# Optimization experiments

Measured on AMD Instinct MI355X. Metric: run time of the kernel, lower is better.

## Reference

```python
import jax, jax.numpy as jnp
import numpy as np

WSCALE = 0.05  # keep ReLU MLP activations in a sane range


def setup_inputs() -> dict:
    key = jax.random.key(0)
    ks = jax.random.split(key, 9)
    B, D, H = 2048, 64, 512
    return {
        "x": jax.random.normal(ks[0], (B, D), dtype=jnp.float32),
        "W1": jax.random.normal(ks[1], (H, D), dtype=jnp.float32) * WSCALE,
        "b1": jax.random.normal(ks[2], (H,), dtype=jnp.float32) * WSCALE,
        "W2": jax.random.normal(ks[3], (H, H), dtype=jnp.float32) * WSCALE,
        "b2": jax.random.normal(ks[4], (H,), dtype=jnp.float32) * WSCALE,
        "W3": jax.random.normal(ks[5], (H, H), dtype=jnp.float32) * WSCALE,
        "b3": jax.random.normal(ks[6], (H,), dtype=jnp.float32) * WSCALE,
        "W4": jax.random.normal(ks[7], (D, H), dtype=jnp.float32) * WSCALE,
        "b4": jax.random.normal(ks[8], (D,), dtype=jnp.float32) * WSCALE,
    }


def reference(x, W1, b1, W2, b2, W3, b3, W4, b4):
    # Score network: ReLU MLP (weights stored PyTorch-style [out, in]).
    a1 = x @ W1.T + b1          # [B, H]
    h1 = jax.nn.relu(a1)
    a2 = h1 @ W2.T + b2
    h2 = jax.nn.relu(a2)
    a3 = h2 @ W3.T + b3
    h3 = jax.nn.relu(a3)
    s = h3 @ W4.T + b4          # [B, D] score

    # Divergence = trace of Jacobian ds/dx per sample.
    # Per-sample J = W4 @ diag(m3) @ W3 @ diag(m2) @ W2 @ diag(m1) @ W1,
    # with m_k = 1[a_k > 0] (ReLU derivative; 0 at 0 like torch autograd).
    m1 = (a1 > 0).astype(x.dtype)
    m2 = (a2 > 0).astype(x.dtype)
    m3 = (a3 > 0).astype(x.dtype)
    T = m1[:, :, None] * W1[None, :, :]                 # [B, H, D]
    T = m2[:, :, None] * jnp.einsum('ij,bjd->bid', W2, T)  # [B, H, D]
    T = m3[:, :, None] * jnp.einsum('ij,bjd->bid', W3, T)  # [B, H, D]
    div = jnp.einsum('dj,bjd->b', W4, T)                # trace of J, [B]

    # Hyvarinen score: 0.5 * ||s||^2 + div
    val = 0.5 * jnp.sum(s * s, axis=1) + div
    return val
```

## Files before the change

### kernel.cpp

```cpp
#include <hip/hip_runtime.h>
#include <stdint.h>


typedef __attribute__((ext_vector_type(8))) short short8;
typedef __attribute__((ext_vector_type(4))) float f32x4;

union U16x8 {
  uint4 u;
  short8 s;
};

__device__ __forceinline__ uint16_t f2bf(float f) {
  uint32_t u = __float_as_uint(f);
  uint32_t lsb = (u >> 16) & 1u;
  u += 0x7FFFu + lsb;
  return (uint16_t)(u >> 16);
}

__device__ __forceinline__ void lds_load16(const uint4* gsrc, uint4* ldst) {
  __builtin_amdgcn_global_load_lds(
      (const __attribute__((address_space(1))) void*)gsrc,
      (__attribute__((address_space(3))) void*)ldst, 16, 0, 0);
}

__global__ __launch_bounds__(256) void convert_kernel(
    const float* __restrict__ W1, const float* __restrict__ W2,
    const float* __restrict__ W3, const float* __restrict__ W4,
    uint16_t* __restrict__ A2swz, uint16_t* __restrict__ A3swz,
    uint16_t* __restrict__ B1swz, uint16_t* __restrict__ B4swz,
    float* __restrict__ W2Tf, float* __restrict__ W3Tf,
    float* __restrict__ W1Tf, float* __restrict__ W4Tf) {
  const int i = blockIdx.x * 256 + threadIdx.x;
  if (i < 262144) {
    const int e = i;
    const int f = e >> 3, j = e & 7;
    const int lane = f & 63, fk = f >> 6;
    const int kc = fk & 15, r16 = fk >> 4;
    const int l15 = lane & 15, quad = lane >> 4;
    const int row = r16 * 16 + l15, col = kc * 32 + quad * 8 + j;
    A2swz[e] = f2bf(W2[row * 512 + col]);
  } else if (i < 524288) {
    const int e = i - 262144;
    const int f = e >> 3, j = e & 7;
    const int lane = f & 63, fk = f >> 6;
    const int kc = fk & 15, r16 = fk >> 4;
    const int l15 = lane & 15, quad = lane >> 4;
    const int row = r16 * 16 + l15, col = kc * 32 + quad * 8 + j;
    A3swz[e] = f2bf(W3[col * 512 + row]);
  } else if (i < 557056) {
    const int e = i - 524288;
    const int f = e >> 3, j = e & 7;
    const int lane = f & 63, fk = f >> 6;
    const int kc = fk >> 2, jt = fk & 3;
    const int l15 = lane & 15, quad = lane >> 4;
    const int d = jt * 16 + l15, col = kc * 32 + quad * 8 + j;
    B1swz[e] = f2bf(W1[col * 64 + d]);
  } else if (i < 589824) {
    const int e = i - 557056;
    const int f = e >> 3, j = e & 7;
    const int lane = f & 63, fk = f >> 6;
    const int kc = fk >> 2, jt = fk & 3;
    const int l15 = lane & 15, quad = lane >> 4;
    const int d = jt * 16 + l15, col = kc * 32 + quad * 8 + j;
    B4swz[e] = f2bf(W4[d * 512 + col]);
  } else if (i < 851968) {
    const int e = i - 589824;
    const int k = e >> 9, jj = e & 511;
    W2Tf[e] = W2[jj * 512 + k];
  } else if (i < 1114112) {
    const int e = i - 851968;
    const int k = e >> 9, jj = e & 511;
    W3Tf[e] = W3[jj * 512 + k];
  } else if (i < 1146880) {
    const int e = i - 1114112;
    const int k = e >> 9, jj = e & 511;
    W1Tf[e] = W1[jj * 64 + k];
  } else if (i < 1179648) {
    const int e = i - 1146880;
    const int k = e >> 6, d = e & 63;
    W4Tf[e] = W4[d * 512 + k];
  }
}

__device__ __forceinline__ float4 frelu4(float a0, float a1, float a2, float a3) {
  float4 r;
  r.x = a0 > 0.f ? a0 : 0.f;
  r.y = a1 > 0.f ? a1 : 0.f;
  r.z = a2 > 0.f ? a2 : 0.f;
  r.w = a3 > 0.f ? a3 : 0.f;
  return r;
}

template <int KPW>
__device__ __forceinline__ void fwd_layer8(
    const float* __restrict__ WT, const float* __restrict__ bias,
    const float4* __restrict__ src, float4* __restrict__ dst,
    float4 (* __restrict__ pa)[512], uint32_t* __restrict__ mbase,
    int t, int lane, int kh) {
  float acc[8][4];
#pragma unroll
  for (int p = 0; p < 8; ++p)
#pragma unroll
    for (int s = 0; s < 4; ++s) acc[p][s] = 0.f;

  const int k0 = kh * KPW;
  const float* Wb = WT + (size_t)k0 * 512 + lane;
  float wA[8], wB[8];
#pragma unroll
  for (int p = 0; p < 8; ++p) wA[p] = Wb[p * 64];
  float4 hA_ = src[k0];

#pragma unroll 1
  for (int kk = 0; kk < KPW; kk += 2) {
    const float4 hB_ = src[k0 + kk + 1];
#pragma unroll
    for (int p = 0; p < 8; ++p) wB[p] = Wb[(size_t)(kk + 1) * 512 + p * 64];
#pragma unroll
    for (int p = 0; p < 8; ++p) {
      acc[p][0] = fmaf(wA[p], hA_.x, acc[p][0]);
      acc[p][1] = fmaf(wA[p], hA_.y, acc[p][1]);
      acc[p][2] = fmaf(wA[p], hA_.z, acc[p][2]);
      acc[p][3] = fmaf(wA[p], hA_.w, acc[p][3]);
    }
    hA_ = src[k0 + kk + 2];
#pragma unroll
    for (int p = 0; p < 8; ++p) wA[p] = Wb[(size_t)(kk + 2) * 512 + p * 64];
#pragma unroll
    for (int p = 0; p < 8; ++p) {
      acc[p][0] = fmaf(wB[p], hB_.x, acc[p][0]);
      acc[p][1] = fmaf(wB[p], hB_.y, acc[p][1]);
      acc[p][2] = fmaf(wB[p], hB_.z, acc[p][2]);
      acc[p][3] = fmaf(wB[p], hB_.w, acc[p][3]);
    }
  }

#pragma unroll
  for (int p = 0; p < 8; ++p) {
    float4 v;
    v.x = acc[p][0]; v.y = acc[p][1]; v.z = acc[p][2]; v.w = acc[p][3];
    pa[kh][p * 64 + lane] = v;
  }
  __syncthreads();

#pragma unroll
  for (int pass = 0; pass < 2; ++pass) {
    const int u = pass * 256 + t;
    const float4 a0 = pa[0][u], a1 = pa[1][u], a2 = pa[2][u], a3 = pa[3][u];
    const float bj = bias[u];
    float a[4];
    a[0] = ((a0.x + a1.x) + (a2.x + a3.x)) + bj;
    a[1] = ((a0.y + a1.y) + (a2.y + a3.y)) + bj;
    a[2] = ((a0.z + a1.z) + (a2.z + a3.z)) + bj;
    a[3] = ((a0.w + a1.w) + (a2.w + a3.w)) + bj;
#pragma unroll
    for (int s = 0; s < 4; ++s) {
      const unsigned long long bal = __ballot(a[s] > 0.f);
      if (lane == 0) {
        uint2 w2;
        w2.x = (uint32_t)bal;
        w2.y = (uint32_t)(bal >> 32);
        *(uint2*)(mbase + (size_t)s * 16 + pass * 8 + 2 * kh) = w2;
      }
    }
    dst[u] = frelu4(a[0], a[1], a[2], a[3]);
  }
  __syncthreads();
}

__global__ __launch_bounds__(256) void forward_kernel(
    const float* __restrict__ x,
    const float* __restrict__ W1Tf, const float* __restrict__ b1,
    const float* __restrict__ W2Tf, const float* __restrict__ b2,
    const float* __restrict__ W3Tf, const float* __restrict__ b3,
    const float* __restrict__ W4Tf, const float* __restrict__ b4,
    uint32_t* __restrict__ m1p, uint32_t* __restrict__ m2p,
    uint32_t* __restrict__ m3p, float* __restrict__ out) {
  __shared__ float4 xs[64];
  __shared__ float4 hU[512];
  __shared__ float4 hV[512];
  __shared__ float4 pa[4][512];
  const int t = threadIdx.x;
  const int lane = t & 63, kh = t >> 6;
  const int b0 = blockIdx.x * 4;

  {
    const int k2 = t >> 2, s2 = t & 3;
    ((float*)&xs[k2])[s2] = x[(size_t)(b0 + s2) * 64 + k2];
  }
  __syncthreads();

  fwd_layer8<16>(W1Tf, b1, xs, hU, pa, m1p + (size_t)b0 * 16, t, lane, kh);
  fwd_layer8<128>(W2Tf, b2, hU, hV, pa, m2p + (size_t)b0 * 16, t, lane, kh);
  fwd_layer8<128>(W3Tf, b3, hV, hU, pa, m3p + (size_t)b0 * 16, t, lane, kh);

  {
    const int d = lane;
    const int k0 = kh * 128;
    const float* Wb = W4Tf + (size_t)k0 * 64 + d;
    float a4[4] = {0.f, 0.f, 0.f, 0.f};
    float wA = Wb[0], wB;
    float4 hA_ = hU[k0], hB_;
#pragma unroll 1
    for (int kk = 0; kk < 128; kk += 2) {
      hB_ = hU[k0 + kk + 1];
      wB = Wb[(size_t)(kk + 1) * 64];
      a4[0] = fmaf(wA, hA_.x, a4[0]); a4[1] = fmaf(wA, hA_.y, a4[1]);
      a4[2] = fmaf(wA, hA_.z, a4[2]); a4[3] = fmaf(wA, hA_.w, a4[3]);
      hA_ = hU[k0 + kk + 2];
      wA = Wb[(size_t)(kk + 2) * 64];
      a4[0] = fmaf(wB, hB_.x, a4[0]); a4[1] = fmaf(wB, hB_.y, a4[1]);
      a4[2] = fmaf(wB, hB_.z, a4[2]); a4[3] = fmaf(wB, hB_.w, a4[3]);
    }
    float4 v;
    v.x = a4[0]; v.y = a4[1]; v.z = a4[2]; v.w = a4[3];
    pa[kh][d] = v;
  }
  __syncthreads();
  if (t < 64) {
    const float4 q0 = pa[0][t], q1 = pa[1][t], q2 = pa[2][t], q3 = pa[3][t];
    const float bj = b4[t];
    float sq[4];
    sq[0] = ((q0.x + q1.x) + (q2.x + q3.x)) + bj;
    sq[1] = ((q0.y + q1.y) + (q2.y + q3.y)) + bj;
    sq[2] = ((q0.z + q1.z) + (q2.z + q3.z)) + bj;
    sq[3] = ((q0.w + q1.w) + (q2.w + q3.w)) + bj;
#pragma unroll
    for (int s = 0; s < 4; ++s) sq[s] *= sq[s];
#pragma unroll
    for (int off = 32; off; off >>= 1) {
      sq[0] += __shfl_down(sq[0], off, 64);
      sq[1] += __shfl_down(sq[1], off, 64);
      sq[2] += __shfl_down(sq[2], off, 64);
      sq[3] += __shfl_down(sq[3], off, 64);
    }
    if (t == 0) {
      out[b0 + 0] = 0.5f * sq[0];
      out[b0 + 1] = 0.5f * sq[1];
      out[b0 + 2] = 0.5f * sq[2];
      out[b0 + 3] = 0.5f * sq[3];
    }
  }
}

__device__ __forceinline__ void expand_mask(uint32_t byte8, uint32_t mk[4]) {
#pragma unroll
  for (int i = 0; i < 4; ++i) {
    mk[i] = (((byte8 >> (2 * i)) & 1u) ? 0x0000FFFFu : 0u) |
            (((byte8 >> (2 * i + 1)) & 1u) ? 0xFFFF0000u : 0u);
  }
}

__global__ __launch_bounds__(512, 4) void div_kernel(
    const uint4* __restrict__ A2swz, const uint4* __restrict__ A3swz,
    const uint4* __restrict__ B1swz, const uint4* __restrict__ B4swz,
    const uint32_t* __restrict__ m1p, const uint32_t* __restrict__ m2p,
    const uint32_t* __restrict__ m3p, float* __restrict__ out) {
  __shared__ uint4 sfrag[3][16][64];
  __shared__ uint4 emask[8][16][4];
  const int t = threadIdx.x;
  const int lane = t & 63, wv = t >> 6;
  const int quad = lane >> 4, l15 = lane & 15;
  const int g4 = blockIdx.x;
  const int rowB0 = blockIdx.y * 64;
  const int sLoc = wv & 3;
  const int b = g4 * 4 + sLoc;
  const int r16b = blockIdx.y * 4;
  const bool isC = (wv < 4);

  const uint4* sb = (wv < 2) ? A2swz : (wv < 4) ? B1swz : (wv < 6) ? A3swz : B4swz;

  f32x4 acc[4][4];
#pragma unroll
  for (int it = 0; it < 4; ++it)
#pragma unroll
    for (int jt = 0; jt < 4; ++jt) acc[it][jt] = (f32x4){0.f, 0.f, 0.f, 0.f};

  {
    const uint32_t* mp = (isC ? m1p : m3p) + (size_t)b * 16;
    const int kcl = lane >> 2, qd = lane & 3;
    const uint32_t word = mp[kcl];
    uint32_t mk[4];
    expand_mask((word >> (qd * 8)) & 0xFFu, mk);
    uint4 v;
    v.x = mk[0]; v.y = mk[1]; v.z = mk[2]; v.w = mk[3];
    emask[wv][kcl][qd] = v;
  }

  auto stage = [&](int sbuf, int kc) {
#pragma unroll
    for (int q = 0; q < 2; ++q) {
      const int sub = (wv & 1) * 2 + q;
      const size_t off = ((wv & 2) == 0)
          ? ((size_t)((r16b + sub) * 16 + kc) * 64 + lane)
          : ((size_t)(kc * 4 + sub) * 64 + lane);
      lds_load16(sb + off, &sfrag[sbuf][wv * 2 + q][0]);
    }
  };

  stage(0, 0);
  stage(1, 1);
  __builtin_amdgcn_sched_barrier(0);
  asm volatile("s_waitcnt vmcnt(2)" ::: "memory");
  __builtin_amdgcn_s_barrier();
  __builtin_amdgcn_sched_barrier(0);

  const int base = isC ? 0 : 8;

#pragma unroll 1
  for (int kc = 0; kc < 16; ++kc) {
    const int rb = kc % 3;
    if (kc < 14) stage((kc + 2) % 3, kc + 2);

    const uint4 mku = emask[wv][kc][quad];

    uint4 a[4], u[4];
#pragma unroll
    for (int q = 0; q < 4; ++q) {
      a[q] = sfrag[rb][base + q][lane];
      u[q] = sfrag[rb][base + 4 + q][lane];
    }

    short8 bf[4];
#pragma unroll
    for (int jt = 0; jt < 4; ++jt) {
      U16x8 uu;
      uu.u = u[jt];
      uu.u.x &= mku.x; uu.u.y &= mku.y; uu.u.z &= mku.z; uu.u.w &= mku.w;
      bf[jt] = uu.s;
    }
#pragma unroll
    for (int it = 0; it < 4; ++it) {
      U16x8 ua;
      ua.u = a[it];
      const short8 af = ua.s;
#pragma unroll
      for (int jt = 0; jt < 4; ++jt)
        acc[it][jt] = __builtin_amdgcn_mfma_f32_16x16x32_bf16(af, bf[jt], acc[it][jt], 0, 0, 0);
    }

    if (kc < 14) {
      asm volatile("s_waitcnt vmcnt(2)" ::: "memory");
    } else if (kc == 14) {
      asm volatile("s_waitcnt vmcnt(0)" ::: "memory");
    }
    if (kc < 15) {
      __builtin_amdgcn_s_barrier();
      __builtin_amdgcn_sched_barrier(0);
    }
  }

  __syncthreads();
  float* cxf = (float*)&sfrag[0][0][0];
  float dsum = 0.f;
  const uint32_t* m2w = m2p + (size_t)b * 16;
#pragma unroll
  for (int h = 0; h < 2; ++h) {
    if (isC) {
#pragma unroll
      for (int ith = 0; ith < 2; ++ith)
#pragma unroll
        for (int jt = 0; jt < 4; ++jt) {
          float* crow = &cxf[((size_t)sLoc * 32 + ith * 16 + quad * 4) * 65 +
                             jt * 16 + l15];
          crow[0 * 65] = acc[h * 2 + ith][jt][0];
          crow[1 * 65] = acc[h * 2 + ith][jt][1];
          crow[2 * 65] = acc[h * 2 + ith][jt][2];
          crow[3 * 65] = acc[h * 2 + ith][jt][3];
        }
    }
    __syncthreads();
    if (!isC) {
#pragma unroll
      for (int ith = 0; ith < 2; ++ith) {
        const int it = h * 2 + ith;
        const int rloc = it * 16 + quad * 4;
        const uint32_t md = m2w[(rowB0 + rloc) >> 5];
        const uint32_t bits = (md >> (rloc & 31)) & 0xFu;
        const float w0 = (bits & 1u) ? 1.f : 0.f;
        const float w1 = (bits & 2u) ? 1.f : 0.f;
        const float w2 = (bits & 4u) ? 1.f : 0.f;
        const float w3 = (bits & 8u) ? 1.f : 0.f;
#pragma unroll
        for (int jt = 0; jt < 4; ++jt) {
          const float* crow = &cxf[((size_t)sLoc * 32 + ith * 16 + quad * 4) * 65 +
                                   jt * 16 + l15];
          dsum = fmaf(w0, acc[it][jt][0] * crow[0 * 65], dsum);
          dsum = fmaf(w1, acc[it][jt][1] * crow[1 * 65], dsum);
          dsum = fmaf(w2, acc[it][jt][2] * crow[2 * 65], dsum);
          dsum = fmaf(w3, acc[it][jt][3] * crow[3 * 65], dsum);
        }
      }
    }
    __syncthreads();
  }
  if (!isC) {
#pragma unroll
    for (int off = 32; off; off >>= 1) dsum += __shfl_down(dsum, off, 64);
    if (lane == 0) atomicAdd(out + b, dsum);
  }
}

extern "C" void kernel_launch(void* const* d_in, const int* in_sizes, int n_in,
                              void* d_out, int out_size, void* d_ws, size_t ws_size,
                              hipStream_t stream) {
  const float* x  = (const float*)d_in[0];
  const float* W1 = (const float*)d_in[1];
  const float* b1 = (const float*)d_in[2];
  const float* W2 = (const float*)d_in[3];
  const float* b2 = (const float*)d_in[4];
  const float* W3 = (const float*)d_in[5];
  const float* b3 = (const float*)d_in[6];
  const float* W4 = (const float*)d_in[7];
  const float* b4 = (const float*)d_in[8];
  float* out = (float*)d_out;

  char* ws = (char*)d_ws;
  uint16_t* A2swz = (uint16_t*)(ws + 0);
  uint16_t* A3swz = (uint16_t*)(ws + 524288);
  uint16_t* B1swz = (uint16_t*)(ws + 1048576);
  uint16_t* B4swz = (uint16_t*)(ws + 1114112);
  float*    W2Tf  = (float*)(ws + 1179648);
  float*    W3Tf  = (float*)(ws + 2228224);
  float*    W1Tf  = (float*)(ws + 3276800);
  float*    W4Tf  = (float*)(ws + 3407872);
  uint32_t* m1p   = (uint32_t*)(ws + 3538944);
  uint32_t* m2p   = (uint32_t*)(ws + 3670016);
  uint32_t* m3p   = (uint32_t*)(ws + 3801088);
  if (ws_size < 3932160) return;

  convert_kernel<<<4608, 256, 0, stream>>>(W1, W2, W3, W4,
                                           A2swz, A3swz, B1swz, B4swz,
                                           W2Tf, W3Tf, W1Tf, W4Tf);
  forward_kernel<<<512, 256, 0, stream>>>(x, W1Tf, b1, W2Tf, b2, W3Tf, b3,
                                          W4Tf, b4, m1p, m2p, m3p, out);
  div_kernel<<<dim3(512, 8), 512, 0, stream>>>((const uint4*)A2swz,
                                               (const uint4*)A3swz,
                                               (const uint4*)B1swz,
                                               (const uint4*)B4swz,
                                               m1p, m2p, m3p, out);
}
```

Measured before the change: 264.4 us.

## Split forward MLP K-reduction across eight waves per block with deeper prefetch

```diff
diff --git a/kernel.cpp b/kernel.cpp
--- a/kernel.cpp
+++ b/kernel.cpp
@@ -82,70 +82,84 @@
   }
 }
 
-__device__ __forceinline__ float4 frelu4(float a0, float a1, float a2, float a3) {
-  float4 r;
-  r.x = a0 > 0.f ? a0 : 0.f;
-  r.y = a1 > 0.f ? a1 : 0.f;
-  r.z = a2 > 0.f ? a2 : 0.f;
-  r.w = a3 > 0.f ? a3 : 0.f;
-  return r;
+__device__ __forceinline__ void fma8x4(float acc[8][4], const float w[8],
+                                       const float4 h) {
+#pragma unroll
+  for (int p = 0; p < 8; ++p) {
+    acc[p][0] = fmaf(w[p], h.x, acc[p][0]);
+    acc[p][1] = fmaf(w[p], h.y, acc[p][1]);
+    acc[p][2] = fmaf(w[p], h.z, acc[p][2]);
+    acc[p][3] = fmaf(w[p], h.w, acc[p][3]);
+  }
 }
 
 template <int KPW>
-__device__ __forceinline__ void fwd_layer8(
+__device__ __forceinline__ void fwd_layer9(
     const float* __restrict__ WT, const float* __restrict__ bias,
     const float4* __restrict__ src, float4* __restrict__ dst,
-    float4 (* __restrict__ pa)[512], uint32_t* __restrict__ mbase,
-    int t, int lane, int kh) {
+    float4 (* __restrict__ pah)[512], uint32_t* __restrict__ mbase,
+    int t, int lane, int wv) {
   float acc[8][4];
 #pragma unroll
   for (int p = 0; p < 8; ++p)
 #pragma unroll
     for (int s = 0; s < 4; ++s) acc[p][s] = 0.f;
 
-  const int k0 = kh * KPW;
+  const int k0 = wv * KPW;
   const float* Wb = WT + (size_t)k0 * 512 + lane;
-  float wA[8], wB[8];
-#pragma unroll
-  for (int p = 0; p < 8; ++p) wA[p] = Wb[p * 64];
-  float4 hA_ = src[k0];
+  float w0[8], w1[8], w2[8], w3[8];
+#pragma unroll
+  for (int p = 0; p < 8; ++p) {
+    w0[p] = Wb[(size_t)0 * 512 + p * 64];
+    w1[p] = Wb[(size_t)1 * 512 + p * 64];
+    w2[p] = Wb[(size_t)2 * 512 + p * 64];
+    w3[p] = Wb[(size_t)3 * 512 + p * 64];
+  }
+  float4 h0 = src[k0 + 0], h1 = src[k0 + 1], h2 = src[k0 + 2], h3 = src[k0 + 3];
 
 #pragma unroll 1
-  for (int kk = 0; kk < KPW; kk += 2) {
-    const float4 hB_ = src[k0 + kk + 1];
-#pragma unroll
-    for (int p = 0; p < 8; ++p) wB[p] = Wb[(size_t)(kk + 1) * 512 + p * 64];
+  for (int kk = 0; kk < KPW; kk += 4) {
+    fma8x4(acc, w0, h0);
+    h0 = src[k0 + kk + 4];
+#pragma unroll
+    for (int p = 0; p < 8; ++p) w0[p] = Wb[(size_t)(kk + 4) * 512 + p * 64];
+    fma8x4(acc, w1, h1);
+    h1 = src[k0 + kk + 5];
+#pragma unroll
+    for (int p = 0; p < 8; ++p) w1[p] = Wb[(size_t)(kk + 5) * 512 + p * 64];
+    fma8x4(acc, w2, h2);
+    h2 = src[k0 + kk + 6];
+#pragma unroll
+    for (int p = 0; p < 8; ++p) w2[p] = Wb[(size_t)(kk + 6) * 512 + p * 64];
+    fma8x4(acc, w3, h3);
+    h3 = src[k0 + kk + 7];
+#pragma unroll
+    for (int p = 0; p < 8; ++p) w3[p] = Wb[(size_t)(kk + 7) * 512 + p * 64];
+  }
+
+  const int half = wv >> 1;
+  if ((wv & 1) == 0) {
 #pragma unroll
     for (int p = 0; p < 8; ++p) {
-      acc[p][0] = fmaf(wA[p], hA_.x, acc[p][0]);
-      acc[p][1] = fmaf(wA[p], hA_.y, acc[p][1]);
-      acc[p][2] = fmaf(wA[p], hA_.z, acc[p][2]);
-      acc[p][3] = fmaf(wA[p], hA_.w, acc[p][3]);
-    }
-    hA_ = src[k0 + kk + 2];
-#pragma unroll
-    for (int p = 0; p < 8; ++p) wA[p] = Wb[(size_t)(kk + 2) * 512 + p * 64];
+      float4 v;
+      v.x = acc[p][0]; v.y = acc[p][1]; v.z = acc[p][2]; v.w = acc[p][3];
+      pah[half][p * 64 + lane] = v;
+    }
+  }
+  __syncthreads();
+  if (wv & 1) {
 #pragma unroll
     for (int p = 0; p < 8; ++p) {
-      acc[p][0] = fmaf(wB[p], hB_.x, acc[p][0]);
-      acc[p][1] = fmaf(wB[p], hB_.y, acc[p][1]);
-      acc[p][2] = fmaf(wB[p], hB_.z, acc[p][2]);
-      acc[p][3] = fmaf(wB[p], hB_.w, acc[p][3]);
-    }
-  }
-
-#pragma unroll
-  for (int p = 0; p < 8; ++p) {
-    float4 v;
-    v.x = acc[p][0]; v.y = acc[p][1]; v.z = acc[p][2]; v.w = acc[p][3];
-    pa[kh][p * 64 + lane] = v;
+      float4 v = pah[half][p * 64 + lane];
+      v.x += acc[p][0]; v.y += acc[p][1]; v.z += acc[p][2]; v.w += acc[p][3];
+      pah[half][p * 64 + lane] = v;
+    }
   }
   __syncthreads();
 
-#pragma unroll
-  for (int pass = 0; pass < 2; ++pass) {
-    const int u = pass * 256 + t;
-    const float4 a0 = pa[0][u], a1 = pa[1][u], a2 = pa[2][u], a3 = pa[3][u];
+  {
+    const int u = t;
+    const float4 a0 = pah[0][u], a1 = pah[1][u], a2 = pah[2][u], a3 = pah[3][u];
     const float bj = bias[u];
     float a[4];
     a[0] = ((a0.x + a1.x) + (a2.x + a3.x)) + bj;
@@ -156,18 +170,23 @@
     for (int s = 0; s < 4; ++s) {
       const unsigned long long bal = __ballot(a[s] > 0.f);
       if (lane == 0) {
-        uint2 w2;
-        w2.x = (uint32_t)bal;
-        w2.y = (uint32_t)(bal >> 32);
-        *(uint2*)(mbase + (size_t)s * 16 + pass * 8 + 2 * kh) = w2;
+        uint2 w2v;
+        w2v.x = (uint32_t)bal;
+        w2v.y = (uint32_t)(bal >> 32);
+        *(uint2*)(mbase + (size_t)s * 16 + 2 * wv) = w2v;
       }
     }
-    dst[u] = frelu4(a[0], a[1], a[2], a[3]);
+    float4 r;
+    r.x = a[0] > 0.f ? a[0] : 0.f;
+    r.y = a[1] > 0.f ? a[1] : 0.f;
+    r.z = a[2] > 0.f ? a[2] : 0.f;
+    r.w = a[3] > 0.f ? a[3] : 0.f;
+    dst[u] = r;
   }
   __syncthreads();
 }
 
-__global__ __launch_bounds__(256) void forward_kernel(
+__global__ __launch_bounds__(512, 4) void forward_kernel(
     const float* __restrict__ x,
     const float* __restrict__ W1Tf, const float* __restrict__ b1,
     const float* __restrict__ W2Tf, const float* __restrict__ b2,
@@ -178,46 +197,62 @@
   __shared__ float4 xs[64];
   __shared__ float4 hU[512];
   __shared__ float4 hV[512];
-  __shared__ float4 pa[4][512];
+  __shared__ float4 pah[4][512];
   const int t = threadIdx.x;
-  const int lane = t & 63, kh = t >> 6;
+  const int lane = t & 63, wv = t >> 6;
   const int b0 = blockIdx.x * 4;
 
-  {
+  if (t < 256) {
     const int k2 = t >> 2, s2 = t & 3;
     ((float*)&xs[k2])[s2] = x[(size_t)(b0 + s2) * 64 + k2];
   }
   __syncthreads();
 
-  fwd_layer8<16>(W1Tf, b1, xs, hU, pa, m1p + (size_t)b0 * 16, t, lane, kh);
-  fwd_layer8<128>(W2Tf, b2, hU, hV, pa, m2p + (size_t)b0 * 16, t, lane, kh);
-  fwd_layer8<128>(W3Tf, b3, hV, hU, pa, m3p + (size_t)b0 * 16, t, lane, kh);
+  fwd_layer9<8>(W1Tf, b1, xs, hU, pah, m1p + (size_t)b0 * 16, t, lane, wv);
+  fwd_layer9<64>(W2Tf, b2, hU, hV, pah, m2p + (size_t)b0 * 16, t, lane, wv);
+  fwd_layer9<64>(W3Tf, b3, hV, hU, pah, m3p + (size_t)b0 * 16, t, lane, wv);
 
   {
     const int d = lane;
-    const int k0 = kh * 128;
-    const float* Wb = W4Tf + (size_t)k0 * 64 + d;
+    const int k0 = wv * 64;
+    const float* Wb4 = W4Tf + (size_t)k0 * 64 + d;
     float a4[4] = {0.f, 0.f, 0.f, 0.f};
-    float wA = Wb[0], wB;
-    float4 hA_ = hU[k0], hB_;
+    float v0 = Wb4[(size_t)0 * 64], v1 = Wb4[(size_t)1 * 64];
+    float v2 = Wb4[(size_t)2 * 64], v3 = Wb4[(size_t)3 * 64];
+    float4 g0 = hU[k0 + 0], g1 = hU[k0 + 1], g2 = hU[k0 + 2], g3 = hU[k0 + 3];
 #pragma unroll 1
-    for (int kk = 0; kk < 128; kk += 2) {
-      hB_ = hU[k0 + kk + 1];
-      wB = Wb[(size_t)(kk + 1) * 64];
-      a4[0] = fmaf(wA, hA_.x, a4[0]); a4[1] = fmaf(wA, hA_.y, a4[1]);
-      a4[2] = fmaf(wA, hA_.z, a4[2]); a4[3] = fmaf(wA, hA_.w, a4[3]);
-      hA_ = hU[k0 + kk + 2];
-      wA = Wb[(size_t)(kk + 2) * 64];
-      a4[0] = fmaf(wB, hB_.x, a4[0]); a4[1] = fmaf(wB, hB_.y, a4[1]);
-      a4[2] = fmaf(wB, hB_.z, a4[2]); a4[3] = fmaf(wB, hB_.w, a4[3]);
-    }
-    float4 v;
-    v.x = a4[0]; v.y = a4[1]; v.z = a4[2]; v.w = a4[3];
-    pa[kh][d] = v;
-  }
-  __syncthreads();
+    for (int kk = 0; kk < 64; kk += 4) {
+      a4[0] = fmaf(v0, g0.x, a4[0]); a4[1] = fmaf(v0, g0.y, a4[1]);
+      a4[2] = fmaf(v0, g0.z, a4[2]); a4[3] = fmaf(v0, g0.w, a4[3]);
+      g0 = hU[k0 + kk + 4];
+      v0 = Wb4[(size_t)(kk + 4) * 64];
+      a4[0] = fmaf(v1, g1.x, a4[0]); a4[1] = fmaf(v1, g1.y, a4[1]);
+      a4[2] = fmaf(v1, g1.z, a4[2]); a4[3] = fmaf(v1, g1.w, a4[3]);
+      g1 = hU[k0 + kk + 5];
+      v1 = Wb4[(size_t)(kk + 5) * 64];
+      a4[0] = fmaf(v2, g2.x, a4[0]); a4[1] = fmaf(v2, g2.y, a4[1]);
+      a4[2] = fmaf(v2, g2.z, a4[2]); a4[3] = fmaf(v2, g2.w, a4[3]);
+      g2 = hU[k0 + kk + 6];
+      v2 = Wb4[(size_t)(kk + 6) * 64];
+      a4[0] = fmaf(v3, g3.x, a4[0]); a4[1] = fmaf(v3, g3.y, a4[1]);
+      a4[2] = fmaf(v3, g3.z, a4[2]); a4[3] = fmaf(v3, g3.w, a4[3]);
+      g3 = hU[k0 + kk + 7];
+      v3 = Wb4[(size_t)(kk + 7) * 64];
+    }
+    const int half = wv >> 1;
+    float4 pv;
+    pv.x = a4[0]; pv.y = a4[1]; pv.z = a4[2]; pv.w = a4[3];
+    if ((wv & 1) == 0) pah[half][d] = pv;
+    __syncthreads();
+    if (wv & 1) {
+      float4 v = pah[half][d];
+      v.x += pv.x; v.y += pv.y; v.z += pv.z; v.w += pv.w;
+      pah[half][d] = v;
+    }
+    __syncthreads();
+  }
   if (t < 64) {
-    const float4 q0 = pa[0][t], q1 = pa[1][t], q2 = pa[2][t], q3 = pa[3][t];
+    const float4 q0 = pah[0][t], q1 = pah[1][t], q2 = pah[2][t], q3 = pah[3][t];
     const float bj = b4[t];
     float sq[4];
     sq[0] = ((q0.x + q1.x) + (q2.x + q3.x)) + bj;
@@ -431,7 +466,7 @@
   convert_kernel<<<4608, 256, 0, stream>>>(W1, W2, W3, W4,
                                            A2swz, A3swz, B1swz, B4swz,
                                            W2Tf, W3Tf, W1Tf, W4Tf);
-  forward_kernel<<<512, 256, 0, stream>>>(x, W1Tf, b1, W2Tf, b2, W3Tf, b3,
+  forward_kernel<<<512, 512, 0, stream>>>(x, W1Tf, b1, W2Tf, b2, W3Tf, b3,
                                           W4Tf, b4, m1p, m2p, m3p, out);
   div_kernel<<<dim3(512, 8), 512, 0, stream>>>((const uint4*)A2swz,
                                                (const uint4*)A3swz,
```

After: 263.0 us. No clear change (-0.5%).
